# Optimization experiments

Measured on AMD Instinct MI355X. Metric: run time of the kernel, lower is better.

## Reference

```python
import jax, jax.numpy as jnp
import numpy as np

B, T, C, H = 8, 2048, 1024, 64

def setup_inputs() -> dict:
    key = jax.random.key(0)
    k1, k2, k3, k4 = jax.random.split(key, 4)
    return {
        "inputs": jax.random.normal(k1, (B, T, C), dtype=jnp.float32),
        "Wq": jax.random.normal(k2, (C, H), dtype=jnp.float32) * (C ** -0.5),
        "Wk": jax.random.normal(k3, (C, H), dtype=jnp.float32) * (C ** -0.5),
        "Wv": jax.random.normal(k4, (C, H), dtype=jnp.float32) * (C ** -0.5),
    }

def reference(inputs, Wq, Wk, Wv):
    # q,k,v: [B,T,H]
    q = jnp.einsum('btc,ch->bth', inputs, Wq)
    k = jnp.einsum('btc,ch->bth', inputs, Wk)
    v = jnp.einsum('btc,ch->bth', inputs, Wv)
    c = inputs.shape[-1]
    # NOTE: original scales by C**-0.5 (embedding dim), not head_size**-0.5
    scale = jnp.asarray(c, inputs.dtype) ** -0.5
    wei = jnp.einsum('bqh,bkh->bqk', q, k) * scale  # [B,T,T]
    t = inputs.shape[1]
    causal = jnp.tril(jnp.ones((t, t), dtype=bool))
    wei = jnp.where(causal[None, :, :], wei, -jnp.inf)
    wei = jax.nn.softmax(wei, axis=-1)
    # dropout is identity in eval / DROP_RATE=0
    out = jnp.einsum('bqk,bkh->bqh', wei, v)  # [B,T,H]
    return out
```

## Files before the change

### kernel.cpp

```cpp
#include <hip/hip_runtime.h>
#include <stdint.h>

#define B_ 8
#define T_ 2048
#define C_ 1024
#define H_ 64
#define M_ (B_*T_)

typedef __bf16 bf16x8 __attribute__((ext_vector_type(8)));
typedef float  f32x4  __attribute__((ext_vector_type(4)));

union U4B { uint4 u; bf16x8 v; };

__device__ __forceinline__ unsigned short f32_to_bf16(float f) {
    union { float f; uint32_t u; } c; c.f = f;
    uint32_t u = c.u;
    u += 0x7fffu + ((u >> 16) & 1u);
    return (unsigned short)(u >> 16);
}
__device__ __forceinline__ uint32_t pack2_bf16(float a, float b) {
#if __has_builtin(__builtin_amdgcn_cvt_pk_bf16_f32)
    typedef __bf16 bf16x2 __attribute__((ext_vector_type(2)));
    union { bf16x2 v; uint32_t u; } c;
    c.v = __builtin_amdgcn_cvt_pk_bf16_f32(a, b);
    return c.u;
#else
    return (uint32_t)f32_to_bf16(a) | ((uint32_t)f32_to_bf16(b) << 16);
#endif
}

__global__ __launch_bounds__(256) void prepack_w(const float* __restrict__ Wq,
        const float* __restrict__ Wk, const float* __restrict__ Wv,
        unsigned short* __restrict__ wpk) {
    int o = blockIdx.x * 256 + threadIdx.x;
    if (o >= 24576) return;
    int lane = o & 63, nt = (o >> 6) % 12, kc = o / (64 * 12);
    int l15 = lane & 15, grp = lane >> 4;
    int n = nt * 16 + l15;
    int k = kc * 32 + grp * 8;
    const float* W = (n < 64) ? Wq : (n < 128) ? Wk : Wv;
    int col = n & 63;
    unsigned short tmp[8];
    #pragma unroll
    for (int j = 0; j < 8; j++) tmp[j] = f32_to_bf16(W[(size_t)(k + j) * 64 + col]);
    *(uint4*)(wpk + (size_t)o * 8) = *(uint4*)tmp;
}

__global__ __launch_bounds__(256) void qkv_kernel(const float* __restrict__ X,
        const unsigned short* __restrict__ wpk,
        unsigned short* __restrict__ qb, unsigned short* __restrict__ kb,
        unsigned short* __restrict__ vt) {
    __shared__ unsigned short Wl[2][12][64][8];
    const int tid = threadIdx.x;
    const int wave = tid >> 6, lane = tid & 63;
    const int grp = lane >> 4, l15 = lane & 15;
    const int i = wave & 1, h = wave >> 1;
    const int t16 = blockIdx.x * 2 + i;

    f32x4 acc[6];
    #pragma unroll
    for (int j = 0; j < 6; j++) acc[j] = (f32x4){0.f, 0.f, 0.f, 0.f};

    const unsigned short* wsrc = wpk + (size_t)tid * 8;
    unsigned short* wdst0 = &Wl[0][0][0][0] + (size_t)tid * 8;
    unsigned short* wdst1 = &Wl[1][0][0][0] + (size_t)tid * 8;

    const float* xp = X + ((size_t)t16 * 16 + l15) * 1024 + grp * 8;

    uint4 w0 = *(const uint4*)(wsrc);
    uint4 w1 = *(const uint4*)(wsrc + 256 * 8);
    uint4 w2 = *(const uint4*)(wsrc + 512 * 8);
    *(uint4*)(wdst0) = w0;
    *(uint4*)(wdst0 + 256 * 8) = w1;
    *(uint4*)(wdst0 + 512 * 8) = w2;
    float4 f0 = *(const float4*)(xp);
    float4 f1 = *(const float4*)(xp + 4);
    U4B a_cur;
    a_cur.u = (uint4){ pack2_bf16(f0.x, f0.y), pack2_bf16(f0.z, f0.w),
                       pack2_bf16(f1.x, f1.y), pack2_bf16(f1.z, f1.w) };
    __syncthreads();

    for (int kc = 0; kc < 32; kc++) {
        const int buf = kc & 1;
        float4 g0, g1;
        if (kc < 31) {
            const unsigned short* wn = wsrc + (size_t)(kc + 1) * 768 * 8;
            w0 = *(const uint4*)(wn);
            w1 = *(const uint4*)(wn + 256 * 8);
            w2 = *(const uint4*)(wn + 512 * 8);
            g0 = *(const float4*)(xp + (kc + 1) * 32);
            g1 = *(const float4*)(xp + (kc + 1) * 32 + 4);
        }
        #pragma unroll
        for (int jj = 0; jj < 6; jj++) {
            bf16x8 bfr = *(const bf16x8*)&Wl[buf][h * 6 + jj][lane][0];
            acc[jj] = __builtin_amdgcn_mfma_f32_16x16x32_bf16(a_cur.v, bfr, acc[jj], 0, 0, 0);
        }
        if (kc < 31) {
            unsigned short* wd = buf ? wdst0 : wdst1;
            *(uint4*)(wd) = w0;
            *(uint4*)(wd + 256 * 8) = w1;
            *(uint4*)(wd + 512 * 8) = w2;
            a_cur.u = (uint4){ pack2_bf16(g0.x, g0.y), pack2_bf16(g0.z, g0.w),
                               pack2_bf16(g1.x, g1.y), pack2_bf16(g1.z, g1.w) };
        }
        __syncthreads();
    }

    const int r0 = t16 * 16 + grp * 4;
    const int bb = r0 >> 11;
    const int t0 = r0 & 2047;
    #pragma unroll
    for (int jj = 0; jj < 6; jj++) {
        int col = (h * 6 + jj) * 16 + l15;
        if (col < 64) {
            for (int r = 0; r < 4; r++)
                qb[(size_t)(r0 + r) * 64 + col] = f32_to_bf16(acc[jj][r] * 0.03125f);
        } else if (col < 128) {
            for (int r = 0; r < 4; r++)
                kb[(size_t)(r0 + r) * 64 + (col - 64)] = f32_to_bf16(acc[jj][r]);
        } else {
            int c = col - 128;
            ushort4 vv;
            vv.x = f32_to_bf16(acc[jj][0]); vv.y = f32_to_bf16(acc[jj][1]);
            vv.z = f32_to_bf16(acc[jj][2]); vv.w = f32_to_bf16(acc[jj][3]);
            *(ushort4*)(vt + ((size_t)bb * 64 + c) * 2048 + t0) = vv;
        }
    }
}

__global__ __launch_bounds__(256) void attn1_kernel(const unsigned short* __restrict__ qb,
        const unsigned short* __restrict__ kb, const unsigned short* __restrict__ vt,
        float* __restrict__ pl, float* __restrict__ pacc) {
    __shared__ unsigned short Kl[64][72];
    __shared__ unsigned short Vl[64][72];
    const int tid = threadIdx.x;
    const int wave = tid >> 6, lane = tid & 63;
    const int grp = lane >> 4, l15 = lane & 15;
    const int b = blockIdx.x & 7;
    int f = blockIdx.x >> 3;
    int g = 0;
    for (; g < 32; g++) { int c = (35 - g) >> 2; if (f < c) break; f -= c; }
    const int j = 31 - g;
    const int s = f;
    const int ktend = min(4, (j + 1) - 4 * s);
    const int qbase = j * 64 + wave * 16;

    const unsigned short* qp = qb + ((size_t)b * 2048 + qbase + l15) * 64 + grp * 8;
    bf16x8 bq0 = *(const bf16x8*)qp;
    bf16x8 bq1 = *(const bf16x8*)(qp + 32);

    float lsum = 0.f;
    f32x4 acc[4];
    for (int d = 0; d < 4; d++) acc[d] = (f32x4){0.f, 0.f, 0.f, 0.f};

    const unsigned short* kB = kb + ((size_t)b * 2048 + s * 256) * 64;
    const unsigned short* vB = vt + (size_t)b * 64 * 2048 + s * 256;
    const int r1 = tid >> 3, c1 = (tid & 7) * 8;
    const int r2 = (tid + 256) >> 3, c2 = c1;

    uint4 kr0, kr1, vr0, vr1;
    kr0 = *(const uint4*)(kB + (size_t)r1 * 64 + c1);
    kr1 = *(const uint4*)(kB + (size_t)r2 * 64 + c2);
    vr0 = *(const uint4*)(vB + (size_t)r1 * 2048 + c1);
    vr1 = *(const uint4*)(vB + (size_t)r2 * 2048 + c2);

    for (int kt = 0; kt < ktend; kt++) {
        *(uint4*)&Kl[r1][c1] = kr0;  *(uint4*)&Kl[r2][c2] = kr1;
        *(uint4*)&Vl[r1][c1] = vr0;  *(uint4*)&Vl[r2][c2] = vr1;
        __syncthreads();
        if (kt + 1 < ktend) {
            const unsigned short* kN = kB + (size_t)(kt + 1) * 64 * 64;
            const unsigned short* vN = vB + (kt + 1) * 64;
            kr0 = *(const uint4*)(kN + (size_t)r1 * 64 + c1);
            kr1 = *(const uint4*)(kN + (size_t)r2 * 64 + c2);
            vr0 = *(const uint4*)(vN + (size_t)r1 * 2048 + c1);
            vr1 = *(const uint4*)(vN + (size_t)r2 * 2048 + c2);
        }
        const int keybase = s * 256 + kt * 64;
        f32x4 st[4];
        #pragma unroll
        for (int nt = 0; nt < 4; nt++) {
            bf16x8 a0 = *(const bf16x8*)&Kl[nt * 16 + l15][grp * 8];
            bf16x8 a1 = *(const bf16x8*)&Kl[nt * 16 + l15][32 + grp * 8];
            f32x4 t = (f32x4){0.f, 0.f, 0.f, 0.f};
            t = __builtin_amdgcn_mfma_f32_16x16x32_bf16(a0, bq0, t, 0, 0, 0);
            t = __builtin_amdgcn_mfma_f32_16x16x32_bf16(a1, bq1, t, 0, 0, 0);
            st[nt] = t;
        }
        if (keybase + 63 > qbase) {
            int q = qbase + l15;
            #pragma unroll
            for (int nt = 0; nt < 4; nt++)
                for (int r = 0; r < 4; r++)
                    if (keybase + nt * 16 + grp * 4 + r > q) st[nt][r] = -1e30f;
        }
        float p[4][4];
        #pragma unroll
        for (int nt = 0; nt < 4; nt++)
            for (int r = 0; r < 4; r++) { p[nt][r] = __expf(st[nt][r]); lsum += p[nt][r]; }
        uint32_t t0a = pack2_bf16(p[0][0], p[0][1]), t0b = pack2_bf16(p[0][2], p[0][3]);
        uint32_t t1a = pack2_bf16(p[1][0], p[1][1]), t1b = pack2_bf16(p[1][2], p[1][3]);
        uint32_t t2a = pack2_bf16(p[2][0], p[2][1]), t2b = pack2_bf16(p[2][2], p[2][3]);
        uint32_t t3a = pack2_bf16(p[3][0], p[3][1]), t3b = pack2_bf16(p[3][2], p[3][3]);
        const int s0l = ((grp & 1) << 5) + l15, s1l = s0l + 16;
        const bool hi = (grp >= 2);
        U4B bw0, bw1;
        {
            uint32_t e0a = (uint32_t)__shfl((int)t0a, s0l, 64);
            uint32_t e0b = (uint32_t)__shfl((int)t0b, s0l, 64);
            uint32_t e0c = (uint32_t)__shfl((int)t0a, s1l, 64);
            uint32_t e0d = (uint32_t)__shfl((int)t0b, s1l, 64);
            uint32_t e1a = (uint32_t)__shfl((int)t1a, s0l, 64);
            uint32_t e1b = (uint32_t)__shfl((int)t1b, s0l, 64);
            uint32_t e1c = (uint32_t)__shfl((int)t1a, s1l, 64);
            uint32_t e1d = (uint32_t)__shfl((int)t1b, s1l, 64);
            bw0.u = (uint4){ hi ? e1a : e0a, hi ? e1b : e0b, hi ? e1c : e0c, hi ? e1d : e0d };
        }
        {
            uint32_t e0a = (uint32_t)__shfl((int)t2a, s0l, 64);
            uint32_t e0b = (uint32_t)__shfl((int)t2b, s0l, 64);
            uint32_t e0c = (uint32_t)__shfl((int)t2a, s1l, 64);
            uint32_t e0d = (uint32_t)__shfl((int)t2b, s1l, 64);
            uint32_t e1a = (uint32_t)__shfl((int)t3a, s0l, 64);
            uint32_t e1b = (uint32_t)__shfl((int)t3b, s0l, 64);
            uint32_t e1c = (uint32_t)__shfl((int)t3a, s1l, 64);
            uint32_t e1d = (uint32_t)__shfl((int)t3b, s1l, 64);
            bw1.u = (uint4){ hi ? e1a : e0a, hi ? e1b : e0b, hi ? e1c : e0c, hi ? e1d : e0d };
        }
        #pragma unroll
        for (int dt = 0; dt < 4; dt++) {
            bf16x8 av0 = *(const bf16x8*)&Vl[dt * 16 + l15][grp * 8];
            bf16x8 av1 = *(const bf16x8*)&Vl[dt * 16 + l15][32 + grp * 8];
            acc[dt] = __builtin_amdgcn_mfma_f32_16x16x32_bf16(av0, bw0.v, acc[dt], 0, 0, 0);
            acc[dt] = __builtin_amdgcn_mfma_f32_16x16x32_bf16(av1, bw1.v, acc[dt], 0, 0, 0);
        }
        __syncthreads();
    }
    lsum += __shfl_xor(lsum, 16, 64);
    lsum += __shfl_xor(lsum, 32, 64);
    size_t rowq = (size_t)b * 2048 + qbase + l15;
    size_t p = rowq * 8 + s;
    if (grp == 0) pl[p] = lsum;
    #pragma unroll
    for (int dt = 0; dt < 4; dt++)
        *(f32x4*)&pacc[p * 64 + dt * 16 + grp * 4] = acc[dt];
}

__global__ __launch_bounds__(256) void attn2_kernel(const float* __restrict__ pl,
        const float* __restrict__ pacc, float* __restrict__ out) {
    int idx = blockIdx.x * 256 + threadIdx.x;
    int row = idx >> 4;
    int d0 = (idx & 15) * 4;
    int t = row & 2047;
    int ns = ((t >> 6) + 4) >> 2;
    float den = 0.f;
    f32x4 num = (f32x4){0.f, 0.f, 0.f, 0.f};
    for (int s = 0; s < ns; s++) {
        den += pl[(size_t)row * 8 + s];
        num += *(const f32x4*)&pacc[((size_t)row * 8 + s) * 64 + d0];
    }
    float inv = 1.f / den;
    *(f32x4*)&out[(size_t)row * 64 + d0] = num * inv;
}

extern "C" void kernel_launch(void* const* d_in, const int* in_sizes, int n_in,
                              void* d_out, int out_size, void* d_ws, size_t ws_size,
                              hipStream_t stream) {
    const float* X  = (const float*)d_in[0];
    const float* Wq = (const float*)d_in[1];
    const float* Wk = (const float*)d_in[2];
    const float* Wv = (const float*)d_in[3];
    float* out = (float*)d_out;

    unsigned short* qb  = (unsigned short*)d_ws;
    unsigned short* kb  = qb + (size_t)M_ * 64;
    unsigned short* wpk = kb + (size_t)M_ * 64;
    unsigned short* vt  = wpk + (size_t)24576 * 8;
    float* pl   = (float*)(vt + (size_t)B_ * 64 * 2048);
    float* pacc = pl + (size_t)M_ * 8;

    prepack_w<<<96, 256, 0, stream>>>(Wq, Wk, Wv, wpk);
    qkv_kernel<<<512, 256, 0, stream>>>(X, wpk, qb, kb, vt);
    attn1_kernel<<<1152, 256, 0, stream>>>(qb, kb, vt, pl, pacc);
    attn2_kernel<<<1024, 256, 0, stream>>>(pl, pacc, out);
}
```

Before: 147.1 us.

## Load QKV weight fragments directly into registers, dropping LDS staging and barriers

The QKV projection kernel no longer stages packed weights through double-buffered shared memory with a barrier every k-step. Each wave loads its own weight fragments from global memory into registers with a one-step prefetch, and prefetches X two steps ahead. Each block now handles one 16-row tile with 3 column tiles per wave, and the grid doubles. This removes synchronisation and LDS traffic at the cost of more redundant L2 reads of the weights.

Measured after the change: 159.6 us. 8.5% more time.

```diff
diff --git a/kernel.cpp b/kernel.cpp
--- a/kernel.cpp
+++ b/kernel.cpp
@@ -50,69 +50,58 @@
         const unsigned short* __restrict__ wpk,
         unsigned short* __restrict__ qb, unsigned short* __restrict__ kb,
         unsigned short* __restrict__ vt) {
-    __shared__ unsigned short Wl[2][12][64][8];
     const int tid = threadIdx.x;
     const int wave = tid >> 6, lane = tid & 63;
     const int grp = lane >> 4, l15 = lane & 15;
-    const int i = wave & 1, h = wave >> 1;
-    const int t16 = blockIdx.x * 2 + i;
-
-    f32x4 acc[6];
-    #pragma unroll
-    for (int j = 0; j < 6; j++) acc[j] = (f32x4){0.f, 0.f, 0.f, 0.f};
-
-    const unsigned short* wsrc = wpk + (size_t)tid * 8;
-    unsigned short* wdst0 = &Wl[0][0][0][0] + (size_t)tid * 8;
-    unsigned short* wdst1 = &Wl[1][0][0][0] + (size_t)tid * 8;
+    const int h = wave;
+    const int t16 = blockIdx.x;
+
+    f32x4 acc[3];
+    #pragma unroll
+    for (int j = 0; j < 3; j++) acc[j] = (f32x4){0.f, 0.f, 0.f, 0.f};
 
     const float* xp = X + ((size_t)t16 * 16 + l15) * 1024 + grp * 8;
-
-    uint4 w0 = *(const uint4*)(wsrc);
-    uint4 w1 = *(const uint4*)(wsrc + 256 * 8);
-    uint4 w2 = *(const uint4*)(wsrc + 512 * 8);
-    *(uint4*)(wdst0) = w0;
-    *(uint4*)(wdst0 + 256 * 8) = w1;
-    *(uint4*)(wdst0 + 512 * 8) = w2;
-    float4 f0 = *(const float4*)(xp);
-    float4 f1 = *(const float4*)(xp + 4);
-    U4B a_cur;
-    a_cur.u = (uint4){ pack2_bf16(f0.x, f0.y), pack2_bf16(f0.z, f0.w),
-                       pack2_bf16(f1.x, f1.y), pack2_bf16(f1.z, f1.w) };
-    __syncthreads();
-
+    const unsigned short* wp = wpk + ((size_t)(h * 3) * 64 + lane) * 8;
+
+    float4 xa0 = *(const float4*)(xp);
+    float4 xb0 = *(const float4*)(xp + 4);
+    float4 xa1 = *(const float4*)(xp + 32);
+    float4 xb1 = *(const float4*)(xp + 36);
+    uint4 wc0 = *(const uint4*)(wp);
+    uint4 wc1 = *(const uint4*)(wp + 64 * 8);
+    uint4 wc2 = *(const uint4*)(wp + 128 * 8);
+
+    #pragma unroll 2
     for (int kc = 0; kc < 32; kc++) {
-        const int buf = kc & 1;
-        float4 g0, g1;
+        U4B a;
+        a.u = (uint4){ pack2_bf16(xa0.x, xa0.y), pack2_bf16(xa0.z, xa0.w),
+                       pack2_bf16(xb0.x, xb0.y), pack2_bf16(xb0.z, xb0.w) };
+        xa0 = xa1; xb0 = xb1;
+        if (kc < 30) {
+            xa1 = *(const float4*)(xp + (kc + 2) * 32);
+            xb1 = *(const float4*)(xp + (kc + 2) * 32 + 4);
+        }
+        uint4 wn0, wn1, wn2;
         if (kc < 31) {
-            const unsigned short* wn = wsrc + (size_t)(kc + 1) * 768 * 8;
-            w0 = *(const uint4*)(wn);
-            w1 = *(const uint4*)(wn + 256 * 8);
-            w2 = *(const uint4*)(wn + 512 * 8);
-            g0 = *(const float4*)(xp + (kc + 1) * 32);
-            g1 = *(const float4*)(xp + (kc + 1) * 32 + 4);
-        }
-        #pragma unroll
-        for (int jj = 0; jj < 6; jj++) {
-            bf16x8 bfr = *(const bf16x8*)&Wl[buf][h * 6 + jj][lane][0];
-            acc[jj] = __builtin_amdgcn_mfma_f32_16x16x32_bf16(a_cur.v, bfr, acc[jj], 0, 0, 0);
-        }
-        if (kc < 31) {
-            unsigned short* wd = buf ? wdst0 : wdst1;
-            *(uint4*)(wd) = w0;
-            *(uint4*)(wd + 256 * 8) = w1;
-            *(uint4*)(wd + 512 * 8) = w2;
-            a_cur.u = (uint4){ pack2_bf16(g0.x, g0.y), pack2_bf16(g0.z, g0.w),
-                               pack2_bf16(g1.x, g1.y), pack2_bf16(g1.z, g1.w) };
-        }
-        __syncthreads();
+            const unsigned short* wn = wp + (size_t)(kc + 1) * 768 * 8;
+            wn0 = *(const uint4*)(wn);
+            wn1 = *(const uint4*)(wn + 64 * 8);
+            wn2 = *(const uint4*)(wn + 128 * 8);
+        }
+        U4B b0, b1, b2;
+        b0.u = wc0; b1.u = wc1; b2.u = wc2;
+        acc[0] = __builtin_amdgcn_mfma_f32_16x16x32_bf16(a.v, b0.v, acc[0], 0, 0, 0);
+        acc[1] = __builtin_amdgcn_mfma_f32_16x16x32_bf16(a.v, b1.v, acc[1], 0, 0, 0);
+        acc[2] = __builtin_amdgcn_mfma_f32_16x16x32_bf16(a.v, b2.v, acc[2], 0, 0, 0);
+        if (kc < 31) { wc0 = wn0; wc1 = wn1; wc2 = wn2; }
     }
 
     const int r0 = t16 * 16 + grp * 4;
     const int bb = r0 >> 11;
     const int t0 = r0 & 2047;
     #pragma unroll
-    for (int jj = 0; jj < 6; jj++) {
-        int col = (h * 6 + jj) * 16 + l15;
+    for (int jj = 0; jj < 3; jj++) {
+        int col = (h * 3 + jj) * 16 + l15;
         if (col < 64) {
             for (int r = 0; r < 4; r++)
                 qb[(size_t)(r0 + r) * 64 + col] = f32_to_bf16(acc[jj][r] * 0.03125f);
@@ -281,7 +270,7 @@
     float* pacc = pl + (size_t)M_ * 8;
 
     prepack_w<<<96, 256, 0, stream>>>(Wq, Wk, Wv, wpk);
-    qkv_kernel<<<512, 256, 0, stream>>>(X, wpk, qb, kb, vt);
+    qkv_kernel<<<1024, 256, 0, stream>>>(X, wpk, qb, kb, vt);
     attn1_kernel<<<1152, 256, 0, stream>>>(qb, kb, vt, pl, pacc);
     attn2_kernel<<<1024, 256, 0, stream>>>(pl, pacc, out);
 }
```
